# Kernel tuning notes

Hardware: AMD Instinct MI355X
Metric: run time of the kernel (lower is better)

Reference implementation:

```python
import jax, jax.numpy as jnp
import numpy as np

C = 256
CQK = C // 8  # query/key channel dim from Conv3d(in, in//8, 1)


def setup_inputs() -> dict:
    key = jax.random.key(0)
    ks = jax.random.split(key, 8)
    B, D, H, W = 2, 16, 16, 16
    x = jax.random.normal(ks[0], (B, C, D, H, W), dtype=jnp.float32)
    s = 1.0 / np.sqrt(C)
    q_w = jax.random.normal(ks[1], (CQK, C), dtype=jnp.float32) * s
    q_b = jax.random.normal(ks[2], (CQK,), dtype=jnp.float32) * 0.01
    k_w = jax.random.normal(ks[3], (CQK, C), dtype=jnp.float32) * s
    k_b = jax.random.normal(ks[4], (CQK,), dtype=jnp.float32) * 0.01
    v_w = jax.random.normal(ks[5], (C, C), dtype=jnp.float32) * s
    v_b = jax.random.normal(ks[6], (C,), dtype=jnp.float32) * 0.01
    gamma = jax.random.normal(ks[7], (1,), dtype=jnp.float32)
    return {"x": x, "q_w": q_w, "q_b": q_b, "k_w": k_w, "k_b": k_b,
            "v_w": v_w, "v_b": v_b, "gamma": gamma}


def reference(x, q_w, q_b, k_w, k_b, v_w, v_b, gamma):
    B, Cc, D, H, W = x.shape
    N = D * H * W
    xf = x.reshape(B, Cc, N)  # [B, C, N]
    # 1x1x1 Conv3d == channel-mixing matmul
    q = jnp.einsum('oc,bcn->bon', q_w, xf) + q_b[None, :, None]  # [B, C/8, N]
    k = jnp.einsum('oc,bcn->bon', k_w, xf) + k_b[None, :, None]  # [B, C/8, N]
    v = jnp.einsum('oc,bcn->bon', v_w, xf) + v_b[None, :, None]  # [B, C, N]
    # attention[b, i, j] = sum_c q[b, c, i] * k[b, c, j]
    attn = jnp.einsum('bci,bcj->bij', q, k)  # [B, N, N]
    attn = jax.nn.softmax(attn, axis=-1)
    # out[b, c, i] = sum_j v[b, c, j] * attn[b, i, j]
    out = jnp.einsum('bcj,bij->bci', v, attn)  # [B, C, N]
    out = out.reshape(B, Cc, D, H, W)
    return gamma[0] * out + x
```

## Files before the change

kernel.cpp:

```cpp
#include <hip/hip_runtime.h>

#define C_DIM 256
#define CQK   32
#define N_DIM 4096
#define B_DIM 2

typedef __attribute__((ext_vector_type(8))) short bf16x8;
typedef __attribute__((ext_vector_type(4))) float f32x4;

__device__ __forceinline__ unsigned short f2bf(float f) {
    union { float f; unsigned u; } v; v.f = f;
    unsigned r = v.u + 0x7FFFu + ((v.u >> 16) & 1u);
    return (unsigned short)(r >> 16);
}
__device__ __forceinline__ unsigned pk2(float a, float b) {
    return (unsigned)f2bf(a) | ((unsigned)f2bf(b) << 16);
}
__device__ __forceinline__ unsigned pk2t(float a, float b) {
    union { float f; unsigned u; } ua, ub; ua.f = a; ub.f = b;
    return __builtin_amdgcn_perm(ub.u, ua.u, 0x07060302u);
}
#define EXP2(x) __builtin_amdgcn_exp2f(x)
#define MFMA(A, B, C) __builtin_amdgcn_mfma_f32_16x16x32_bf16((A), (B), (C), 0, 0, 0)

__global__ __launch_bounds__(256) void wconv(
    const float* __restrict__ q_w, const float* __restrict__ q_b,
    const float* __restrict__ k_w, const float* __restrict__ k_b,
    const float* __restrict__ v_w, const float* __restrict__ v_b,
    unsigned short* __restrict__ wbf, float* __restrict__ biasf)
{
    const float LOG2E = 1.4426950408889634f;
    int o = blockIdx.x, c = threadIdx.x;
    float w;
    if (o < 32)       w = q_w[o * C_DIM + c] * LOG2E;
    else if (o < 64)  w = k_w[(o - 32) * C_DIM + c];
    else              w = v_w[(o - 64) * C_DIM + c];
    wbf[o * C_DIM + c] = f2bf(w);
    if (c == 0) biasf[o] = (o < 32) ? q_b[o] * LOG2E
                         : (o < 64) ? k_b[o - 32] : v_b[o - 64];
}

__global__ __launch_bounds__(256, 2) void qkv_proj(
    const float* __restrict__ x, const unsigned short* __restrict__ wbf,
    const float* __restrict__ biasf,
    unsigned short* __restrict__ qT, unsigned short* __restrict__ kT,
    unsigned short* __restrict__ vbf)
{
    __shared__ __align__(16) unsigned short xsT[16 * 264];
    __shared__ __align__(16) unsigned short qkbuf[2][16 * 36];
    __shared__ __align__(16) unsigned short vbb[256 * 20];
    const int t  = threadIdx.x;
    const int b  = blockIdx.x >> 8;
    const int n0 = (blockIdx.x & 255) * 16;

    {
        int n4 = t & 3, cq = t >> 2;
        const float* xp = x + ((size_t)(b * C_DIM + cq * 4)) * N_DIM + n0 + n4 * 4;
        float4 r0 = *(const float4*)xp;
        float4 r1 = *(const float4*)(xp + N_DIM);
        float4 r2 = *(const float4*)(xp + 2 * N_DIM);
        float4 r3 = *(const float4*)(xp + 3 * N_DIM);
        float a0[4], a1[4], a2[4], a3[4];
        *(float4*)a0 = r0; *(float4*)a1 = r1; *(float4*)a2 = r2; *(float4*)a3 = r3;
        #pragma unroll
        for (int k = 0; k < 4; ++k) {
            uint2 pw;
            pw.x = pk2(a0[k], a1[k]);
            pw.y = pk2(a2[k], a3[k]);
            *(uint2*)&xsT[(n4 * 4 + k) * 264 + cq * 4] = pw;
        }
    }
    __syncthreads();

    const int w = t >> 6, lid = t & 63, lr = lid & 15, lq = lid >> 4;
    f32x4 acc[5] = {};
    #pragma unroll
    for (int ks = 0; ks < 8; ++ks) {
        bf16x8 xb = *(const bf16x8*)&xsT[lr * 264 + ks * 32 + lq * 8];
        #pragma unroll
        for (int u = 0; u < 5; ++u) {
            int gm = w * 5 + u;
            bf16x8 af = *(const bf16x8*)&wbf[(gm * 16 + lr) * C_DIM + ks * 32 + lq * 8];
            acc[u] = MFMA(af, xb, acc[u]);
        }
    }
    #pragma unroll
    for (int u = 0; u < 5; ++u) {
        int gm = w * 5 + u;
        float bv[4];
        *(float4*)bv = *(const float4*)&biasf[gm * 16 + lq * 4];
        if (gm >= 4) {
            int vc = (gm - 4) * 16 + lq * 4;
            #pragma unroll
            for (int r = 0; r < 4; ++r)
                vbb[(vc + r) * 20 + lr] = f2bf(acc[u][r] + bv[r]);
        } else {
            int sel = gm >> 1, half = gm & 1;
            uint2 pw;
            pw.x = pk2(acc[u][0] + bv[0], acc[u][1] + bv[1]);
            pw.y = pk2(acc[u][2] + bv[2], acc[u][3] + bv[3]);
            *(uint2*)&qkbuf[sel][lr * 36 + half * 16 + lq * 4] = pw;
        }
    }
    __syncthreads();
    if (t < 128) {
        int sel = t >> 6, idx = t & 63;
        int n = idx >> 2, ch8 = (idx & 3) * 8;
        const unsigned short* src = &qkbuf[sel][n * 36 + ch8];
        uint2 a = *(const uint2*)src;
        uint2 c = *(const uint2*)(src + 4);
        unsigned short* dst = (sel ? kT : qT) + ((size_t)b * N_DIM + n0 + n) * CQK + ch8;
        uint4 st; st.x = a.x; st.y = a.y; st.z = c.x; st.w = c.y;
        *(uint4*)dst = st;
    }
    {
        const unsigned short* src = &vbb[t * 20];
        uint2 a = *(const uint2*)(src + 0);
        uint2 bq = *(const uint2*)(src + 4);
        uint2 c = *(const uint2*)(src + 8);
        uint2 d = *(const uint2*)(src + 12);
        unsigned short* dst = vbf + ((size_t)b * C_DIM + t) * N_DIM + n0;
        uint4 s0; s0.x = a.x; s0.y = a.y; s0.z = bq.x; s0.w = bq.y;
        uint4 s1; s1.x = c.x; s1.y = c.y; s1.z = d.x; s1.w = d.y;
        *(uint4*)dst = s0;
        *(uint4*)(dst + 8) = s1;
    }
}

__global__ __launch_bounds__(256, 2) void attn_kernel(
    const unsigned short* __restrict__ qT, const unsigned short* __restrict__ kT,
    const unsigned short* __restrict__ vbf, const float* __restrict__ x,
    const float* __restrict__ gamma, float* __restrict__ out)
{
    __shared__ __align__(16) char smem[20480 + 1280];
    unsigned short* pbase = (unsigned short*)smem;
    float* obuf = (float*)smem;
    float* lbuf = (float*)(smem + 20480);

    const int t  = threadIdx.x;
    const int b  = blockIdx.x >> 8;
    const int qt = (blockIdx.x >> 2) & 63;
    const int cs = blockIdx.x & 3;
    const int i0 = qt * 64, c0 = cs * 64;
    const int w = t >> 6, lid = t & 63, lr = lid & 15, lq = lid >> 4;

    const unsigned short* qTb = qT + (size_t)b * N_DIM * CQK;
    const unsigned short* kTb = kT + (size_t)b * N_DIM * CQK;
    const unsigned short* vb  = vbf + (size_t)b * C_DIM * N_DIM;

    unsigned short* pW = pbase + w * (64 * 40);

    bf16x8 bq[4];
    #pragma unroll
    for (int it = 0; it < 4; ++it)
        bq[it] = *(const bf16x8*)&qTb[(i0 + it * 16 + lr) * CQK + lq * 8];

    f32x4 oa[4][4] = {};
    float lp[4] = {};

    const int jwbase = w * 1024;
    bf16x8 ak0 = *(const bf16x8*)&kTb[(jwbase + lr) * CQK + lq * 8];
    bf16x8 ak1 = *(const bf16x8*)&kTb[(jwbase + 16 + lr) * CQK + lq * 8];
    bf16x8 av[4];
    #pragma unroll
    for (int ct = 0; ct < 4; ++ct)
        av[ct] = *(const bf16x8*)&vb[(size_t)(c0 + ct * 16 + lr) * N_DIM + jwbase + lq * 8];

    #pragma unroll 2
    for (int jj = 0; jj < 1024; jj += 32) {
        const int jn = jwbase + ((jj + 32) & 1023);
        bf16x8 ak0n = *(const bf16x8*)&kTb[(jn + lr) * CQK + lq * 8];
        bf16x8 ak1n = *(const bf16x8*)&kTb[(jn + 16 + lr) * CQK + lq * 8];
        bf16x8 avn[4];
        #pragma unroll
        for (int ct = 0; ct < 4; ++ct)
            avn[ct] = *(const bf16x8*)&vb[(size_t)(c0 + ct * 16 + lr) * N_DIM + jn + lq * 8];

        const f32x4 z = {};
        #pragma unroll
        for (int it = 0; it < 4; ++it) {
            f32x4 s0 = MFMA(ak0, bq[it], z);
            f32x4 s1 = MFMA(ak1, bq[it], z);
            float e0 = EXP2(s0[0]), e1 = EXP2(s0[1]), e2 = EXP2(s0[2]), e3 = EXP2(s0[3]);
            float f0 = EXP2(s1[0]), f1 = EXP2(s1[1]), f2 = EXP2(s1[2]), f3 = EXP2(s1[3]);
            lp[it] += ((e0 + e1) + (e2 + e3)) + ((f0 + f1) + (f2 + f3));
            uint2 pw0; pw0.x = pk2t(e0, e1); pw0.y = pk2t(e2, e3);
            uint2 pw1; pw1.x = pk2t(f0, f1); pw1.y = pk2t(f2, f3);
            unsigned short* prow = pW + (it * 16 + lr) * 40;
            *(uint2*)&prow[lq * 4]      = pw0;
            *(uint2*)&prow[16 + lq * 4] = pw1;
        }
        __asm__ __volatile__("" ::: "memory");
        #pragma unroll
        for (int it = 0; it < 4; ++it) {
            bf16x8 bp = *(const bf16x8*)&pW[(it * 16 + lr) * 40 + lq * 8];
            #pragma unroll
            for (int ct = 0; ct < 4; ++ct)
                oa[ct][it] = MFMA(av[ct], bp, oa[ct][it]);
        }
        ak0 = ak0n; ak1 = ak1n;
        #pragma unroll
        for (int ct = 0; ct < 4; ++ct) av[ct] = avn[ct];
    }

    #pragma unroll
    for (int it = 0; it < 4; ++it) {
        lp[it] += __shfl_xor(lp[it], 16);
        lp[it] += __shfl_xor(lp[it], 32);
    }
    if (lq == 0) {
        #pragma unroll
        for (int it = 0; it < 4; ++it)
            lbuf[w * 64 + it * 16 + lr] = lp[it];
    }
    __syncthreads();

    for (int ph = 0; ph < 4; ++ph) {
        if (w == ph) {
            #pragma unroll
            for (int ct = 0; ct < 4; ++ct)
                #pragma unroll
                for (int it = 0; it < 4; ++it)
                    #pragma unroll
                    for (int r = 0; r < 4; ++r) {
                        int addr = (ct * 16 + lq * 4 + r) * 68 + it * 16 + lr;
                        if (ph == 0) obuf[addr]  = oa[ct][it][r];
                        else         obuf[addr] += oa[ct][it][r];
                    }
        }
        __syncthreads();
    }
    if (t < 64) {
        float l = lbuf[t] + lbuf[64 + t] + lbuf[128 + t] + lbuf[192 + t];
        lbuf[256 + t] = 1.f / l;
    }
    __syncthreads();

    const float g = gamma[0];
    const int cc = t >> 2;
    const int ic = (t & 3) * 16;
    const size_t rowbase = ((size_t)b * C_DIM + c0 + cc) * N_DIM + i0 + ic;
    #pragma unroll
    for (int k = 0; k < 4; ++k) {
        float4 ov4 = *(const float4*)&obuf[cc * 68 + ic + k * 4];
        float4 li  = *(const float4*)&lbuf[256 + ic + k * 4];
        float4 xv  = *(const float4*)(x + rowbase + k * 4);
        float4 ov;
        ov.x = g * ov4.x * li.x + xv.x;
        ov.y = g * ov4.y * li.y + xv.y;
        ov.z = g * ov4.z * li.z + xv.z;
        ov.w = g * ov4.w * li.w + xv.w;
        *(float4*)(out + rowbase + k * 4) = ov;
    }
}

extern "C" void kernel_launch(void* const* d_in, const int* in_sizes, int n_in,
                              void* d_out, int out_size, void* d_ws, size_t ws_size,
                              hipStream_t stream) {
    const float* x     = (const float*)d_in[0];
    const float* q_w   = (const float*)d_in[1];
    const float* q_b   = (const float*)d_in[2];
    const float* k_w   = (const float*)d_in[3];
    const float* k_b   = (const float*)d_in[4];
    const float* v_w   = (const float*)d_in[5];
    const float* v_b   = (const float*)d_in[6];
    const float* gamma = (const float*)d_in[7];
    float* out = (float*)d_out;

    char* ws = (char*)d_ws;
    unsigned short* qT    = (unsigned short*)(ws);
    unsigned short* kT    = (unsigned short*)(ws + 524288);
    unsigned short* vbf   = (unsigned short*)(ws + 1048576);
    unsigned short* wbf   = (unsigned short*)(ws + 5242880);
    float*          biasf = (float*)(ws + 5406720);

    hipLaunchKernelGGL(wconv, dim3(320), dim3(256), 0, stream,
                       q_w, q_b, k_w, k_b, v_w, v_b, wbf, biasf);
    hipLaunchKernelGGL(qkv_proj, dim3(B_DIM * 256), dim3(256), 0, stream,
                       x, wbf, biasf, qT, kT, vbf);
    hipLaunchKernelGGL(attn_kernel, dim3(B_DIM * 64 * 4), dim3(256), 0, stream,
                       qT, kT, vbf, x, gamma, out);
}
```

Measured before the change: 134.4 us.

## Software-pipeline QK exp and PV MFMA across iterations with double-buffered P

Restructures the attention inner loop so each iteration computes the QK scores and exp for tile k while running the PV MFMAs on tile k-1's probabilities, which are read from a second LDS buffer. A prologue and epilogue handle the first and last tiles. The aim is to overlap the transcendental/VALU work with matrix-core work and to hide the LDS write-to-read latency. In exchange, LDS use per block doubles to about 42KB and register pressure rises, which may cut occupancy at launch bounds of 2 blocks.

```diff
diff --git a/kernel.cpp b/kernel.cpp
--- a/kernel.cpp
+++ b/kernel.cpp
@@ -132,10 +132,10 @@
     const unsigned short* __restrict__ vbf, const float* __restrict__ x,
     const float* __restrict__ gamma, float* __restrict__ out)
 {
-    __shared__ __align__(16) char smem[20480 + 1280];
+    __shared__ __align__(16) char smem[40960 + 1536];
     unsigned short* pbase = (unsigned short*)smem;
     float* obuf = (float*)smem;
-    float* lbuf = (float*)(smem + 20480);
+    float* lbuf = (float*)(smem + 40960);
 
     const int t  = threadIdx.x;
     const int b  = blockIdx.x >> 8;
@@ -148,7 +148,8 @@
     const unsigned short* kTb = kT + (size_t)b * N_DIM * CQK;
     const unsigned short* vb  = vbf + (size_t)b * C_DIM * N_DIM;
 
-    unsigned short* pW = pbase + w * (64 * 40);
+    unsigned short* pW0 = pbase + (w * 2 + 0) * (64 * 40);
+    unsigned short* pW1 = pbase + (w * 2 + 1) * (64 * 40);
 
     bf16x8 bq[4];
     #pragma unroll
@@ -159,48 +160,90 @@
     float lp[4] = {};
 
     const int jwbase = w * 1024;
-    bf16x8 ak0 = *(const bf16x8*)&kTb[(jwbase + lr) * CQK + lq * 8];
-    bf16x8 ak1 = *(const bf16x8*)&kTb[(jwbase + 16 + lr) * CQK + lq * 8];
-    bf16x8 av[4];
-    #pragma unroll
-    for (int ct = 0; ct < 4; ++ct)
-        av[ct] = *(const bf16x8*)&vb[(size_t)(c0 + ct * 16 + lr) * N_DIM + jwbase + lq * 8];
-
-    #pragma unroll 2
-    for (int jj = 0; jj < 1024; jj += 32) {
-        const int jn = jwbase + ((jj + 32) & 1023);
-        bf16x8 ak0n = *(const bf16x8*)&kTb[(jn + lr) * CQK + lq * 8];
-        bf16x8 ak1n = *(const bf16x8*)&kTb[(jn + 16 + lr) * CQK + lq * 8];
-        bf16x8 avn[4];
+
+    bf16x8 akc0 = *(const bf16x8*)&kTb[(jwbase + lr) * CQK + lq * 8];
+    bf16x8 akc1 = *(const bf16x8*)&kTb[(jwbase + 16 + lr) * CQK + lq * 8];
+    bf16x8 avU[4];
+
+    {
         #pragma unroll
         for (int ct = 0; ct < 4; ++ct)
-            avn[ct] = *(const bf16x8*)&vb[(size_t)(c0 + ct * 16 + lr) * N_DIM + jn + lq * 8];
-
+            avU[ct] = *(const bf16x8*)&vb[(size_t)(c0 + ct * 16 + lr) * N_DIM + jwbase + lq * 8];
+        bf16x8 akn0 = *(const bf16x8*)&kTb[(jwbase + 32 + lr) * CQK + lq * 8];
+        bf16x8 akn1 = *(const bf16x8*)&kTb[(jwbase + 32 + 16 + lr) * CQK + lq * 8];
         const f32x4 z = {};
         #pragma unroll
         for (int it = 0; it < 4; ++it) {
-            f32x4 s0 = MFMA(ak0, bq[it], z);
-            f32x4 s1 = MFMA(ak1, bq[it], z);
+            f32x4 s0 = MFMA(akc0, bq[it], z);
+            f32x4 s1 = MFMA(akc1, bq[it], z);
             float e0 = EXP2(s0[0]), e1 = EXP2(s0[1]), e2 = EXP2(s0[2]), e3 = EXP2(s0[3]);
             float f0 = EXP2(s1[0]), f1 = EXP2(s1[1]), f2 = EXP2(s1[2]), f3 = EXP2(s1[3]);
             lp[it] += ((e0 + e1) + (e2 + e3)) + ((f0 + f1) + (f2 + f3));
             uint2 pw0; pw0.x = pk2t(e0, e1); pw0.y = pk2t(e2, e3);
             uint2 pw1; pw1.x = pk2t(f0, f1); pw1.y = pk2t(f2, f3);
-            unsigned short* prow = pW + (it * 16 + lr) * 40;
+            unsigned short* prow = pW0 + (it * 16 + lr) * 40;
             *(uint2*)&prow[lq * 4]      = pw0;
             *(uint2*)&prow[16 + lq * 4] = pw1;
         }
-        __asm__ __volatile__("" ::: "memory");
+        akc0 = akn0; akc1 = akn1;
+    }
+
+    #pragma unroll 2
+    for (int k = 1; k < 32; ++k) {
+        const int j0 = jwbase + k * 32;
+        const int jn = jwbase + ((k + 1) & 31) * 32;
+        bf16x8 avI[4];
+        #pragma unroll
+        for (int ct = 0; ct < 4; ++ct)
+            avI[ct] = *(const bf16x8*)&vb[(size_t)(c0 + ct * 16 + lr) * N_DIM + j0 + lq * 8];
+        bf16x8 akn0 = *(const bf16x8*)&kTb[(jn + lr) * CQK + lq * 8];
+        bf16x8 akn1 = *(const bf16x8*)&kTb[(jn + 16 + lr) * CQK + lq * 8];
+        const unsigned short* pR = (k & 1) ? pW0 : pW1;
+        bf16x8 bp[4];
+        #pragma unroll
+        for (int it = 0; it < 4; ++it)
+            bp[it] = *(const bf16x8*)&pR[(it * 16 + lr) * 40 + lq * 8];
+        const f32x4 z = {};
+        f32x4 s[4][2];
         #pragma unroll
         for (int it = 0; it < 4; ++it) {
-            bf16x8 bp = *(const bf16x8*)&pW[(it * 16 + lr) * 40 + lq * 8];
+            s[it][0] = MFMA(akc0, bq[it], z);
+            s[it][1] = MFMA(akc1, bq[it], z);
+        }
+        #pragma unroll
+        for (int it = 0; it < 4; ++it)
             #pragma unroll
             for (int ct = 0; ct < 4; ++ct)
-                oa[ct][it] = MFMA(av[ct], bp, oa[ct][it]);
-        }
-        ak0 = ak0n; ak1 = ak1n;
-        #pragma unroll
-        for (int ct = 0; ct < 4; ++ct) av[ct] = avn[ct];
+                oa[ct][it] = MFMA(avU[ct], bp[it], oa[ct][it]);
+        unsigned short* pWc = (k & 1) ? pW1 : pW0;
+        #pragma unroll
+        for (int it = 0; it < 4; ++it) {
+            float e0 = EXP2(s[it][0][0]), e1 = EXP2(s[it][0][1]);
+            float e2 = EXP2(s[it][0][2]), e3 = EXP2(s[it][0][3]);
+            float f0 = EXP2(s[it][1][0]), f1 = EXP2(s[it][1][1]);
+            float f2 = EXP2(s[it][1][2]), f3 = EXP2(s[it][1][3]);
+            lp[it] += ((e0 + e1) + (e2 + e3)) + ((f0 + f1) + (f2 + f3));
+            uint2 pw0; pw0.x = pk2t(e0, e1); pw0.y = pk2t(e2, e3);
+            uint2 pw1; pw1.x = pk2t(f0, f1); pw1.y = pk2t(f2, f3);
+            unsigned short* prow = pWc + (it * 16 + lr) * 40;
+            *(uint2*)&prow[lq * 4]      = pw0;
+            *(uint2*)&prow[16 + lq * 4] = pw1;
+        }
+        akc0 = akn0; akc1 = akn1;
+        #pragma unroll
+        for (int ct = 0; ct < 4; ++ct) avU[ct] = avI[ct];
+    }
+
+    {
+        bf16x8 bp[4];
+        #pragma unroll
+        for (int it = 0; it < 4; ++it)
+            bp[it] = *(const bf16x8*)&pW1[(it * 16 + lr) * 40 + lq * 8];
+        #pragma unroll
+        for (int it = 0; it < 4; ++it)
+            #pragma unroll
+            for (int ct = 0; ct < 4; ++ct)
+                oa[ct][it] = MFMA(avU[ct], bp[it], oa[ct][it]);
     }
 
     #pragma unroll
```

Result: no change. 132.1 us (-1.7%).

## Software-pipeline attention loop with double-buffered P tiles across 64-key steps

Applied to the files above, without the earlier changes.

Restructures the per-wave key loop to process 64 keys per step and software-pipeline it. The QK^T MFMAs and exp for the current tile overlap the PV MFMAs for the previous tile, whose probabilities sit in a second LDS buffer. This is meant to hide MFMA-to-exp dependency latency and LDS round-trip latency within a wave. The cost is LDS use growing from about 21KB to 75KB per block, which may limit occupancy below the launch-bounds target of two blocks, plus much higher register pressure from the s[4][4] and avU/avI arrays.

```diff
diff --git a/kernel.cpp b/kernel.cpp
--- a/kernel.cpp
+++ b/kernel.cpp
@@ -132,10 +132,10 @@
     const unsigned short* __restrict__ vbf, const float* __restrict__ x,
     const float* __restrict__ gamma, float* __restrict__ out)
 {
-    __shared__ __align__(16) char smem[20480 + 1280];
+    __shared__ __align__(16) char smem[73728 + 1536];
     unsigned short* pbase = (unsigned short*)smem;
     float* obuf = (float*)smem;
-    float* lbuf = (float*)(smem + 20480);
+    float* lbuf = (float*)(smem + 73728);
 
     const int t  = threadIdx.x;
     const int b  = blockIdx.x >> 8;
@@ -148,7 +148,8 @@
     const unsigned short* kTb = kT + (size_t)b * N_DIM * CQK;
     const unsigned short* vb  = vbf + (size_t)b * C_DIM * N_DIM;
 
-    unsigned short* pW = pbase + w * (64 * 40);
+    unsigned short* pW0 = pbase + (w * 2 + 0) * (64 * 72);
+    unsigned short* pW1 = pbase + (w * 2 + 1) * (64 * 72);
 
     bf16x8 bq[4];
     #pragma unroll
@@ -159,48 +160,113 @@
     float lp[4] = {};
 
     const int jwbase = w * 1024;
-    bf16x8 ak0 = *(const bf16x8*)&kTb[(jwbase + lr) * CQK + lq * 8];
-    bf16x8 ak1 = *(const bf16x8*)&kTb[(jwbase + 16 + lr) * CQK + lq * 8];
-    bf16x8 av[4];
-    #pragma unroll
-    for (int ct = 0; ct < 4; ++ct)
-        av[ct] = *(const bf16x8*)&vb[(size_t)(c0 + ct * 16 + lr) * N_DIM + jwbase + lq * 8];
-
-    #pragma unroll 2
-    for (int jj = 0; jj < 1024; jj += 32) {
-        const int jn = jwbase + ((jj + 32) & 1023);
-        bf16x8 ak0n = *(const bf16x8*)&kTb[(jn + lr) * CQK + lq * 8];
-        bf16x8 ak1n = *(const bf16x8*)&kTb[(jn + 16 + lr) * CQK + lq * 8];
-        bf16x8 avn[4];
+
+    bf16x8 akc[4];
+    #pragma unroll
+    for (int jt = 0; jt < 4; ++jt)
+        akc[jt] = *(const bf16x8*)&kTb[(jwbase + jt * 16 + lr) * CQK + lq * 8];
+    bf16x8 avU[4][2];
+
+    {
         #pragma unroll
         for (int ct = 0; ct < 4; ++ct)
-            avn[ct] = *(const bf16x8*)&vb[(size_t)(c0 + ct * 16 + lr) * N_DIM + jn + lq * 8];
-
+            #pragma unroll
+            for (int ks = 0; ks < 2; ++ks)
+                avU[ct][ks] = *(const bf16x8*)&vb[(size_t)(c0 + ct * 16 + lr) * N_DIM
+                                                  + jwbase + ks * 32 + lq * 8];
+        bf16x8 akn[4];
+        #pragma unroll
+        for (int jt = 0; jt < 4; ++jt)
+            akn[jt] = *(const bf16x8*)&kTb[(jwbase + 64 + jt * 16 + lr) * CQK + lq * 8];
         const f32x4 z = {};
-        #pragma unroll
-        for (int it = 0; it < 4; ++it) {
-            f32x4 s0 = MFMA(ak0, bq[it], z);
-            f32x4 s1 = MFMA(ak1, bq[it], z);
-            float e0 = EXP2(s0[0]), e1 = EXP2(s0[1]), e2 = EXP2(s0[2]), e3 = EXP2(s0[3]);
-            float f0 = EXP2(s1[0]), f1 = EXP2(s1[1]), f2 = EXP2(s1[2]), f3 = EXP2(s1[3]);
-            lp[it] += ((e0 + e1) + (e2 + e3)) + ((f0 + f1) + (f2 + f3));
-            uint2 pw0; pw0.x = pk2t(e0, e1); pw0.y = pk2t(e2, e3);
-            uint2 pw1; pw1.x = pk2t(f0, f1); pw1.y = pk2t(f2, f3);
-            unsigned short* prow = pW + (it * 16 + lr) * 40;
-            *(uint2*)&prow[lq * 4]      = pw0;
-            *(uint2*)&prow[16 + lq * 4] = pw1;
-        }
-        __asm__ __volatile__("" ::: "memory");
-        #pragma unroll
-        for (int it = 0; it < 4; ++it) {
-            bf16x8 bp = *(const bf16x8*)&pW[(it * 16 + lr) * 40 + lq * 8];
+        f32x4 s[4][4];
+        #pragma unroll
+        for (int jt = 0; jt < 4; ++jt)
+            #pragma unroll
+            for (int it = 0; it < 4; ++it)
+                s[jt][it] = MFMA(akc[jt], bq[it], z);
+        #pragma unroll
+        for (int jt = 0; jt < 4; ++jt)
+            #pragma unroll
+            for (int it = 0; it < 4; ++it) {
+                float e0 = EXP2(s[jt][it][0]), e1 = EXP2(s[jt][it][1]);
+                float e2 = EXP2(s[jt][it][2]), e3 = EXP2(s[jt][it][3]);
+                lp[it] += (e0 + e1) + (e2 + e3);
+                uint2 pw; pw.x = pk2t(e0, e1); pw.y = pk2t(e2, e3);
+                *(uint2*)&pW0[(it * 16 + lr) * 72 + jt * 16 + lq * 4] = pw;
+            }
+        #pragma unroll
+        for (int jt = 0; jt < 4; ++jt) akc[jt] = akn[jt];
+    }
+
+    for (int k = 1; k < 16; ++k) {
+        const int j0 = jwbase + k * 64;
+        const int jn = jwbase + ((k + 1) & 15) * 64;
+        bf16x8 avI[4][2];
+        #pragma unroll
+        for (int ct = 0; ct < 4; ++ct)
+            #pragma unroll
+            for (int ks = 0; ks < 2; ++ks)
+                avI[ct][ks] = *(const bf16x8*)&vb[(size_t)(c0 + ct * 16 + lr) * N_DIM
+                                                  + j0 + ks * 32 + lq * 8];
+        bf16x8 akn[4];
+        #pragma unroll
+        for (int jt = 0; jt < 4; ++jt)
+            akn[jt] = *(const bf16x8*)&kTb[(jn + jt * 16 + lr) * CQK + lq * 8];
+        const unsigned short* pR = (k & 1) ? pW0 : pW1;
+        bf16x8 bp[4][2];
+        #pragma unroll
+        for (int it = 0; it < 4; ++it)
+            #pragma unroll
+            for (int ks = 0; ks < 2; ++ks)
+                bp[it][ks] = *(const bf16x8*)&pR[(it * 16 + lr) * 72 + ks * 32 + lq * 8];
+        const f32x4 z = {};
+        f32x4 s[4][4];
+        #pragma unroll
+        for (int jt = 0; jt < 4; ++jt)
+            #pragma unroll
+            for (int it = 0; it < 4; ++it)
+                s[jt][it] = MFMA(akc[jt], bq[it], z);
+        #pragma unroll
+        for (int it = 0; it < 4; ++it)
             #pragma unroll
             for (int ct = 0; ct < 4; ++ct)
-                oa[ct][it] = MFMA(av[ct], bp, oa[ct][it]);
-        }
-        ak0 = ak0n; ak1 = ak1n;
-        #pragma unroll
-        for (int ct = 0; ct < 4; ++ct) av[ct] = avn[ct];
+                #pragma unroll
+                for (int ks = 0; ks < 2; ++ks)
+                    oa[ct][it] = MFMA(avU[ct][ks], bp[it][ks], oa[ct][it]);
+        unsigned short* pWc = (k & 1) ? pW1 : pW0;
+        #pragma unroll
+        for (int jt = 0; jt < 4; ++jt)
+            #pragma unroll
+            for (int it = 0; it < 4; ++it) {
+                float e0 = EXP2(s[jt][it][0]), e1 = EXP2(s[jt][it][1]);
+                float e2 = EXP2(s[jt][it][2]), e3 = EXP2(s[jt][it][3]);
+                lp[it] += (e0 + e1) + (e2 + e3);
+                uint2 pw; pw.x = pk2t(e0, e1); pw.y = pk2t(e2, e3);
+                *(uint2*)&pWc[(it * 16 + lr) * 72 + jt * 16 + lq * 4] = pw;
+            }
+        #pragma unroll
+        for (int jt = 0; jt < 4; ++jt) akc[jt] = akn[jt];
+        #pragma unroll
+        for (int ct = 0; ct < 4; ++ct)
+            #pragma unroll
+            for (int ks = 0; ks < 2; ++ks) avU[ct][ks] = avI[ct][ks];
+    }
+
+    {
+        bf16x8 bp[4][2];
+        #pragma unroll
+        for (int it = 0; it < 4; ++it)
+            #pragma unroll
+            for (int ks = 0; ks < 2; ++ks)
+                bp[it][ks] = *(const bf16x8*)&pW1[(it * 16 + lr) * 72 + ks * 32 + lq * 8];
+        #pragma unroll
+        for (int it = 0; it < 4; ++it)
+            #pragma unroll
+            for (int ct = 0; ct < 4; ++ct)
+                #pragma unroll
+                for (int ks = 0; ks < 2; ++ks)
+                    oa[ct][it] = MFMA(avU[ct][ks], bp[it][ks], oa[ct][it]);
     }
 
     #pragma unroll
```

New measurement: 134.0 us. About the same (-0.3%).
